# Kernel optimization log

Measured on AMD Instinct MI355X. Metric: run time of the kernel, lower is better.

The kernel has to match this reference:

```python
import jax, jax.numpy as jnp
import numpy as np

P = 8  # patch_size hard-coded in the module


def conv1x1(x, W, b):
    # x: [B,C,H,W_], W: [O,C], b: [O]  (1x1 conv == per-pixel linear)
    return jnp.einsum('oc,bchw->bohw', W, x) + b[None, :, None, None]


def to_patch_tokens(t):
    # Replicates t.unfold(2,P,P).unfold(3,P,P).contiguous().view(B,-1,N)
    # t: [B,Cq,W,H] -> [B, Cq*P*P, N] with N = (W//P)*(H//P)
    B, Cq, Wd, Hd = t.shape
    Wp, Hp = Wd // P, Hd // P
    t = t.reshape(B, Cq, Wp, P, Hp, P).transpose(0, 1, 2, 4, 3, 5)  # [B,Cq,Wp,Hp,P,P]
    return t.reshape(B, Cq * P * P, Wp * Hp)


def setup_inputs() -> dict:
    key = jax.random.key(0)
    ks = jax.random.split(key, 10)
    B, C, Wd, Hd = 8, 64, 256, 256
    Cq = C // 8
    s_in = 1.0 / np.sqrt(C)
    s_out = 1.0 / np.sqrt(Cq)
    return {
        'x': jax.random.normal(ks[0], (B, C, Wd, Hd), jnp.float32),
        'Wq': jax.random.normal(ks[1], (Cq, C), jnp.float32) * s_in,
        'bq': jax.random.normal(ks[2], (Cq,), jnp.float32) * 0.01,
        'Wk': jax.random.normal(ks[3], (Cq, C), jnp.float32) * s_in,
        'bk': jax.random.normal(ks[4], (Cq,), jnp.float32) * 0.01,
        'Wv': jax.random.normal(ks[5], (Cq, C), jnp.float32) * s_in,
        'bv': jax.random.normal(ks[6], (Cq,), jnp.float32) * 0.01,
        'Wo': jax.random.normal(ks[7], (C, Cq), jnp.float32) * s_out,
        'bo': jax.random.normal(ks[8], (C,), jnp.float32) * 0.01,
        'gamma': jax.random.normal(ks[9], (1,), jnp.float32),
    }


def reference(x, Wq, bq, Wk, bk, Wv, bv, Wo, bo, gamma):
    B, C, Wd, Hd = x.shape
    Cq = C // 8
    q = to_patch_tokens(conv1x1(x, Wq, bq)).transpose(0, 2, 1)  # [B,N,M]
    k = to_patch_tokens(conv1x1(x, Wk, bk))                     # [B,M,N]
    v = to_patch_tokens(conv1x1(x, Wv, bv))                     # [B,M,N]
    N = k.shape[-1]  # d_k in source == number of patch tokens
    energy = jnp.einsum('bnm,bmk->bnk', q, k) / jnp.sqrt(jnp.float32(N))
    attn = jax.nn.softmax(energy, axis=-1)                      # [B,N,N]
    out = jnp.einsum('bmn,bjn->bmj', v, attn)                   # bmm(v, attn^T)
    out = out.transpose(0, 2, 1).reshape(B, Cq, Wd, Hd)
    out = conv1x1(out, Wo, bo)
    return gamma * out + x
```

## Files before the change

### kernel.cpp

```cpp
#include <hip/hip_runtime.h>
#include <stdint.h>

typedef unsigned short u16;
typedef unsigned int   u32;
typedef __attribute__((ext_vector_type(8))) short  short8;
typedef __attribute__((ext_vector_type(4))) float  floatx4;

__device__ __forceinline__ u16 f32_to_bf16(float f) {
  u32 u = __builtin_bit_cast(u32, f);
  u = (u + 0x7fffu + ((u >> 16) & 1u)) >> 16;
  return (u16)u;
}
__device__ __forceinline__ float bf16_to_f32(u16 h) {
  u32 u = ((u32)h) << 16;
  return __builtin_bit_cast(float, u);
}

__device__ __forceinline__ void load_lds16(const u16* g, u16* l) {
  auto gp = (const __attribute__((address_space(1))) u32*)(uintptr_t)g;
  auto lp = (__attribute__((address_space(3))) u32*)(u32)(uintptr_t)l;
  __builtin_amdgcn_global_load_lds(gp, lp, 16, 0, 0);
}

__global__ __launch_bounds__(1024) void qkv_kernel(
    const float* __restrict__ x,
    const float* __restrict__ Wq, const float* __restrict__ bq,
    const float* __restrict__ Wk, const float* __restrict__ bk,
    const float* __restrict__ Wv, const float* __restrict__ bv,
    u16* __restrict__ qt, u16* __restrict__ kt, u16* __restrict__ vm)
{
  __shared__ __align__(16) u16 qs[128 * 64];
  __shared__ __align__(16) u16 ks_[128 * 64];
  __shared__ __align__(16) u16 vs[64 * 128];

  const int wq = blockIdx.x;
  const int g  = blockIdx.y;
  const int b  = blockIdx.z;
  const int t  = threadIdx.x;
  const int lw = t >> 5, lh = t & 31;
  const int w  = wq * 32 + lw;
  const int h  = g * 16 + (lh & 15) + ((lh >> 4) << 7);
  const int nl = ((lh >> 3) & 1) * 64 + (lw & 7) * 8 + (lh & 7);
  const int mc = ((lw >> 3) << 1) + (lh >> 4);

  float aq[8], ak[8], av[8];
#pragma unroll
  for (int i = 0; i < 8; i++) { aq[i] = 0.f; ak[i] = 0.f; av[i] = 0.f; }

  const float* xp = x + (size_t)b * 64 * 65536 + w * 256 + h;
#pragma unroll 4
  for (int c = 0; c < 64; c++) {
    float xv = xp[c * 65536];
#pragma unroll
    for (int cq = 0; cq < 8; cq++) {
      aq[cq] = fmaf(Wq[cq * 64 + c], xv, aq[cq]);
      ak[cq] = fmaf(Wk[cq * 64 + c], xv, ak[cq]);
      av[cq] = fmaf(Wv[cq * 64 + c], xv, av[cq]);
    }
  }
#pragma unroll
  for (int cq = 0; cq < 8; cq++) {
    qs[nl * 64 + cq * 8 + mc]  = f32_to_bf16(aq[cq] + bq[cq]);
    ks_[nl * 64 + cq * 8 + mc] = f32_to_bf16(ak[cq] + bk[cq]);
    vs[(cq * 8 + mc) * 128 + nl] = f32_to_bf16(av[cq] + bv[cq]);
  }
  __syncthreads();

  {
    const int nl2 = t >> 3, cq2 = t & 7;
    const size_t row = (size_t)b * 1024 + g * 128 + nl2;
    uint4 vq = *(const uint4*)(qs + nl2 * 64 + cq2 * 8);
    uint4 vk = *(const uint4*)(ks_ + nl2 * 64 + cq2 * 8);
    *(uint4*)(qt + row * 512 + cq2 * 64 + wq * 8) = vq;
    *(uint4*)(kt + row * 512 + cq2 * 64 + wq * 8) = vk;
  }
  {
    const int pr = t >> 4, l16 = t & 15;
    const int cq3 = pr >> 3, mc3 = pr & 7;
    const int mrow = cq3 * 64 + wq * 8 + mc3;
    uint4 vv = *(const uint4*)(vs + pr * 128 + l16 * 8);
    *(uint4*)(vm + ((size_t)b * 512 + mrow) * 1024 + g * 128 + l16 * 8) = vv;
  }
}

template <int FMW>
__global__ __launch_bounds__(256) void gemm_nt(
    const u16* __restrict__ A, const u16* __restrict__ Bm, u16* __restrict__ Cm,
    int M, int N, int K, float scale)
{
  constexpr int BM = FMW * 32;
  __shared__ __align__(16) u16 As[BM * 64];
  __shared__ __align__(16) u16 Bs[128 * 64];

  const int bn = blockIdx.x, bm = blockIdx.y, bz = blockIdx.z;
  const int t = threadIdx.x;
  const int lane = t & 63, wid = t >> 6;
  const int wm = wid & 1, wn = wid >> 1;
  const int m0 = bm * BM, n0 = bn * 128;

  const u16* Ab = A + (size_t)bz * M * K + (size_t)m0 * K;
  const u16* Bb = Bm + (size_t)bz * N * K + (size_t)n0 * K;

  floatx4 acc[FMW][4];
#pragma unroll
  for (int i = 0; i < FMW; i++)
#pragma unroll
    for (int j = 0; j < 4; j++) acc[i][j] = (floatx4){0.f, 0.f, 0.f, 0.f};

  const int srow = wid * 8 + (lane >> 3);
  const int scol = (((lane & 7) ^ ((lane >> 3) & 7)) << 3);
  const int l15 = lane & 15, quad = lane >> 4;
  const int cxor = (l15 & 7) << 3;

  for (int k0 = 0; k0 < K; k0 += 64) {
#pragma unroll
    for (int i = 0; i < FMW; i++)
      load_lds16(Ab + (size_t)(i * 32 + srow) * K + k0 + scol, As + (i * 32 + wid * 8) * 64);
#pragma unroll
    for (int i = 0; i < 4; i++)
      load_lds16(Bb + (size_t)(i * 32 + srow) * K + k0 + scol, Bs + (i * 32 + wid * 8) * 64);
    __syncthreads();
#pragma unroll
    for (int ks = 0; ks < 2; ks++) {
      const int koff = (ks * 32 + quad * 8) ^ cxor;
      short8 a[FMW], b[4];
#pragma unroll
      for (int f = 0; f < FMW; f++)
        a[f] = *(const short8*)(As + (wm * FMW * 16 + f * 16 + l15) * 64 + koff);
#pragma unroll
      for (int f = 0; f < 4; f++)
        b[f] = *(const short8*)(Bs + (wn * 64 + f * 16 + l15) * 64 + koff);
#pragma unroll
      for (int fm = 0; fm < FMW; fm++)
#pragma unroll
        for (int fn = 0; fn < 4; fn++)
          acc[fm][fn] = __builtin_amdgcn_mfma_f32_16x16x32_bf16(a[fm], b[fn], acc[fm][fn], 0, 0, 0);
    }
    __syncthreads();
  }

  u16* Cb = Cm + (size_t)bz * M * N;
#pragma unroll
  for (int fm = 0; fm < FMW; fm++)
#pragma unroll
    for (int fn = 0; fn < 4; fn++)
#pragma unroll
      for (int r = 0; r < 4; r++) {
        int row = m0 + wm * FMW * 16 + fm * 16 + quad * 4 + r;
        int col = n0 + wn * 64 + fn * 16 + l15;
        Cb[(size_t)row * N + col] = f32_to_bf16(scale * acc[fm][fn][r]);
      }
}

__global__ __launch_bounds__(256) void softmax_kernel(u16* __restrict__ EP)
{
  const int r = blockIdx.x;
  u16* row = EP + (size_t)r * 1024;
  const int t = threadIdx.x;
  const int lane = t & 63, wid = t >> 6;

  ushort4 hv = ((const ushort4*)row)[t];
  float e[4] = {bf16_to_f32(hv.x), bf16_to_f32(hv.y), bf16_to_f32(hv.z), bf16_to_f32(hv.w)};

  float mx = fmaxf(fmaxf(e[0], e[1]), fmaxf(e[2], e[3]));
#pragma unroll
  for (int off = 32; off > 0; off >>= 1) mx = fmaxf(mx, __shfl_xor(mx, off));
  __shared__ float redm[4];
  if (lane == 0) redm[wid] = mx;
  __syncthreads();
  mx = fmaxf(fmaxf(redm[0], redm[1]), fmaxf(redm[2], redm[3]));

  float s = 0.f;
#pragma unroll
  for (int i = 0; i < 4; i++) { e[i] = __expf(e[i] - mx); s += e[i]; }
#pragma unroll
  for (int off = 32; off > 0; off >>= 1) s += __shfl_xor(s, off);
  __shared__ float reds[4];
  if (lane == 0) reds[wid] = s;
  __syncthreads();
  s = reds[0] + reds[1] + reds[2] + reds[3];

  float inv = 1.0f / s;
  hv.x = f32_to_bf16(e[0] * inv);
  hv.y = f32_to_bf16(e[1] * inv);
  hv.z = f32_to_bf16(e[2] * inv);
  hv.w = f32_to_bf16(e[3] * inv);
  ((ushort4*)row)[t] = hv;
}

__global__ __launch_bounds__(256) void out_kernel(
    const float* __restrict__ x, const u16* __restrict__ OT,
    const float* __restrict__ Wo, const float* __restrict__ bo,
    const float* __restrict__ gammap, float* __restrict__ out)
{
  const int pix = blockIdx.x * 256 + threadIdx.x;
  const int b = pix >> 16, rem = pix & 65535;
  const float g = gammap[0];

  const u16* otb = OT + (size_t)b * 524288;
  const int m = rem & 511;
  const int nbase = rem >> 9;
  float oc[8];
#pragma unroll
  for (int cq = 0; cq < 8; cq++)
    oc[cq] = bf16_to_f32(otb[(size_t)(cq * 128 + nbase) * 512 + m]);

  const float* xb = x + (size_t)b * 4194304 + rem;
  float* ob = out + (size_t)b * 4194304 + rem;
#pragma unroll 4
  for (int o = 0; o < 64; o++) {
    float acc = bo[o];
#pragma unroll
    for (int cq = 0; cq < 8; cq++) acc = fmaf(Wo[o * 8 + cq], oc[cq], acc);
    ob[o * 65536] = fmaf(g, acc, xb[o * 65536]);
  }
}

extern "C" void kernel_launch(void* const* d_in, const int* in_sizes, int n_in,
                              void* d_out, int out_size, void* d_ws, size_t ws_size,
                              hipStream_t stream) {
  const float* x  = (const float*)d_in[0];
  const float* Wq = (const float*)d_in[1];
  const float* bq = (const float*)d_in[2];
  const float* Wk = (const float*)d_in[3];
  const float* bk = (const float*)d_in[4];
  const float* Wv = (const float*)d_in[5];
  const float* bv = (const float*)d_in[6];
  const float* Wo = (const float*)d_in[7];
  const float* bo = (const float*)d_in[8];
  const float* gm = (const float*)d_in[9];
  float* out = (float*)d_out;

  u16* qt = (u16*)d_ws;
  u16* kt = qt + 4194304;
  u16* vm = kt + 4194304;
  u16* EP = vm + 4194304;
  u16* OT = qt;

  qkv_kernel<<<dim3(8, 8, 8), 1024, 0, stream>>>(x, Wq, bq, Wk, bk, Wv, bv, qt, kt, vm);
  gemm_nt<4><<<dim3(8, 8, 8), 256, 0, stream>>>(qt, kt, EP, 1024, 1024, 512, 0.03125f);
  softmax_kernel<<<8192, 256, 0, stream>>>(EP);
  gemm_nt<2><<<dim3(4, 16, 8), 256, 0, stream>>>(EP, vm, OT, 1024, 512, 1024, 1.0f);
  out_kernel<<<2048, 256, 0, stream>>>(x, OT, Wo, bo, gm, out);
}
```

Before: 340.7 us.

## Fuse five kernels into one persistent kernel with software grid barriers

Replaces the five separate launches with a single persistent kernel of 512 blocks that runs the QKV, energy GEMM, softmax, PV GEMM and output phases in turn, separated by atomic-counter grid barriers. The goal is to remove launch gaps and kernel-boundary drain between stages. The QKV phase now uses 256 threads looping four times, and the first GEMM switches to a 64-row tile done twice per block. This relies on all 512 blocks being co-resident, which could deadlock if occupancy is too low, and the barrier spinning plus reduced per-phase parallelism may cost throughput.

```diff
diff --git a/kernel.cpp b/kernel.cpp
--- a/kernel.cpp
+++ b/kernel.cpp
@@ -22,88 +22,105 @@
   __builtin_amdgcn_global_load_lds(gp, lp, 16, 0, 0);
 }
 
-__global__ __launch_bounds__(1024) void qkv_kernel(
-    const float* __restrict__ x,
+__global__ void init_ctr(u32* ctr) { if (threadIdx.x < 16) ctr[threadIdx.x] = 0; }
+
+__device__ __forceinline__ void grid_barrier(u32* ctr, u32 target) {
+  __syncthreads();
+  if (threadIdx.x == 0) {
+    __threadfence();
+    __hip_atomic_fetch_add(ctr, 1u, __ATOMIC_ACQ_REL, __HIP_MEMORY_SCOPE_AGENT);
+    while (__hip_atomic_load(ctr, __ATOMIC_ACQUIRE, __HIP_MEMORY_SCOPE_AGENT) < target)
+      __builtin_amdgcn_s_sleep(2);
+    __threadfence();
+  }
+  __syncthreads();
+}
+
+__device__ __forceinline__ void qkv_phase(
+    char* pool, int bx, int t, const float* __restrict__ x,
     const float* __restrict__ Wq, const float* __restrict__ bq,
     const float* __restrict__ Wk, const float* __restrict__ bk,
     const float* __restrict__ Wv, const float* __restrict__ bv,
     u16* __restrict__ qt, u16* __restrict__ kt, u16* __restrict__ vm)
 {
-  __shared__ __align__(16) u16 qs[128 * 64];
-  __shared__ __align__(16) u16 ks_[128 * 64];
-  __shared__ __align__(16) u16 vs[64 * 128];
-
-  const int wq = blockIdx.x;
-  const int g  = blockIdx.y;
-  const int b  = blockIdx.z;
-  const int t  = threadIdx.x;
-  const int lw = t >> 5, lh = t & 31;
-  const int w  = wq * 32 + lw;
-  const int h  = g * 16 + (lh & 15) + ((lh >> 4) << 7);
-  const int nl = ((lh >> 3) & 1) * 64 + (lw & 7) * 8 + (lh & 7);
-  const int mc = ((lw >> 3) << 1) + (lh >> 4);
-
-  float aq[8], ak[8], av[8];
-#pragma unroll
-  for (int i = 0; i < 8; i++) { aq[i] = 0.f; ak[i] = 0.f; av[i] = 0.f; }
-
-  const float* xp = x + (size_t)b * 64 * 65536 + w * 256 + h;
+  u16* qs  = (u16*)pool;
+  u16* ks_ = qs + 8192;
+  u16* vs  = ks_ + 8192;
+
+  const int wq = bx & 7, g = (bx >> 3) & 7, b = bx >> 6;
+
+#pragma unroll
+  for (int i = 0; i < 4; i++) {
+    const int vt = t + i * 256;
+    const int lw = vt >> 5, lh = vt & 31;
+    const int w  = wq * 32 + lw;
+    const int h  = g * 16 + (lh & 15) + ((lh >> 4) << 7);
+    const int nl = ((lh >> 3) & 1) * 64 + (lw & 7) * 8 + (lh & 7);
+    const int mc = ((lw >> 3) << 1) + (lh >> 4);
+
+    float aq[8], ak[8], av[8];
+#pragma unroll
+    for (int j = 0; j < 8; j++) { aq[j] = 0.f; ak[j] = 0.f; av[j] = 0.f; }
+
+    const float* xp = x + (size_t)b * 64 * 65536 + w * 256 + h;
 #pragma unroll 4
-  for (int c = 0; c < 64; c++) {
-    float xv = xp[c * 65536];
+    for (int c = 0; c < 64; c++) {
+      float xv = xp[c * 65536];
+#pragma unroll
+      for (int cq = 0; cq < 8; cq++) {
+        aq[cq] = fmaf(Wq[cq * 64 + c], xv, aq[cq]);
+        ak[cq] = fmaf(Wk[cq * 64 + c], xv, ak[cq]);
+        av[cq] = fmaf(Wv[cq * 64 + c], xv, av[cq]);
+      }
+    }
 #pragma unroll
     for (int cq = 0; cq < 8; cq++) {
-      aq[cq] = fmaf(Wq[cq * 64 + c], xv, aq[cq]);
-      ak[cq] = fmaf(Wk[cq * 64 + c], xv, ak[cq]);
-      av[cq] = fmaf(Wv[cq * 64 + c], xv, av[cq]);
-    }
-  }
-#pragma unroll
-  for (int cq = 0; cq < 8; cq++) {
-    qs[nl * 64 + cq * 8 + mc]  = f32_to_bf16(aq[cq] + bq[cq]);
-    ks_[nl * 64 + cq * 8 + mc] = f32_to_bf16(ak[cq] + bk[cq]);
-    vs[(cq * 8 + mc) * 128 + nl] = f32_to_bf16(av[cq] + bv[cq]);
-  }
-  __syncthreads();
-
-  {
-    const int nl2 = t >> 3, cq2 = t & 7;
-    const size_t row = (size_t)b * 1024 + g * 128 + nl2;
-    uint4 vq = *(const uint4*)(qs + nl2 * 64 + cq2 * 8);
-    uint4 vk = *(const uint4*)(ks_ + nl2 * 64 + cq2 * 8);
-    *(uint4*)(qt + row * 512 + cq2 * 64 + wq * 8) = vq;
-    *(uint4*)(kt + row * 512 + cq2 * 64 + wq * 8) = vk;
-  }
-  {
-    const int pr = t >> 4, l16 = t & 15;
-    const int cq3 = pr >> 3, mc3 = pr & 7;
-    const int mrow = cq3 * 64 + wq * 8 + mc3;
-    uint4 vv = *(const uint4*)(vs + pr * 128 + l16 * 8);
-    *(uint4*)(vm + ((size_t)b * 512 + mrow) * 1024 + g * 128 + l16 * 8) = vv;
-  }
-}
-
-template <int FMW>
-__global__ __launch_bounds__(256) void gemm_nt(
+      qs[nl * 64 + cq * 8 + mc]    = f32_to_bf16(aq[cq] + bq[cq]);
+      ks_[nl * 64 + cq * 8 + mc]   = f32_to_bf16(ak[cq] + bk[cq]);
+      vs[(cq * 8 + mc) * 128 + nl] = f32_to_bf16(av[cq] + bv[cq]);
+    }
+  }
+  __syncthreads();
+
+#pragma unroll
+  for (int i = 0; i < 4; i++) {
+    const int vt = t + i * 256;
+    {
+      const int nl2 = vt >> 3, cq2 = vt & 7;
+      const size_t row = (size_t)b * 1024 + g * 128 + nl2;
+      uint4 vq = *(const uint4*)(qs + nl2 * 64 + cq2 * 8);
+      uint4 vk = *(const uint4*)(ks_ + nl2 * 64 + cq2 * 8);
+      *(uint4*)(qt + row * 512 + cq2 * 64 + wq * 8) = vq;
+      *(uint4*)(kt + row * 512 + cq2 * 64 + wq * 8) = vk;
+    }
+    {
+      const int pr = vt >> 4, l16 = vt & 15;
+      const int cq3 = pr >> 3, mc3 = pr & 7;
+      const int mrow = cq3 * 64 + wq * 8 + mc3;
+      uint4 vv = *(const uint4*)(vs + pr * 128 + l16 * 8);
+      *(uint4*)(vm + ((size_t)b * 512 + mrow) * 1024 + g * 128 + l16 * 8) = vv;
+    }
+  }
+}
+
+__device__ __forceinline__ void gemm_phase(
+    char* pool, int t,
     const u16* __restrict__ A, const u16* __restrict__ Bm, u16* __restrict__ Cm,
-    int M, int N, int K, float scale)
-{
-  constexpr int BM = FMW * 32;
-  __shared__ __align__(16) u16 As[BM * 64];
-  __shared__ __align__(16) u16 Bs[128 * 64];
-
-  const int bn = blockIdx.x, bm = blockIdx.y, bz = blockIdx.z;
-  const int t = threadIdx.x;
+    int M, int N, int K, float scale, int bm, int bn, int bz)
+{
+  u16* As = (u16*)pool;
+  u16* Bs = As + 4096;
+
   const int lane = t & 63, wid = t >> 6;
   const int wm = wid & 1, wn = wid >> 1;
-  const int m0 = bm * BM, n0 = bn * 128;
+  const int m0 = bm * 64, n0 = bn * 128;
 
   const u16* Ab = A + (size_t)bz * M * K + (size_t)m0 * K;
   const u16* Bb = Bm + (size_t)bz * N * K + (size_t)n0 * K;
 
-  floatx4 acc[FMW][4];
-#pragma unroll
-  for (int i = 0; i < FMW; i++)
+  floatx4 acc[2][4];
+#pragma unroll
+  for (int i = 0; i < 2; i++)
 #pragma unroll
     for (int j = 0; j < 4; j++) acc[i][j] = (floatx4){0.f, 0.f, 0.f, 0.f};
 
@@ -114,7 +131,7 @@
 
   for (int k0 = 0; k0 < K; k0 += 64) {
 #pragma unroll
-    for (int i = 0; i < FMW; i++)
+    for (int i = 0; i < 2; i++)
       load_lds16(Ab + (size_t)(i * 32 + srow) * K + k0 + scol, As + (i * 32 + wid * 8) * 64);
 #pragma unroll
     for (int i = 0; i < 4; i++)
@@ -123,15 +140,15 @@
 #pragma unroll
     for (int ks = 0; ks < 2; ks++) {
       const int koff = (ks * 32 + quad * 8) ^ cxor;
-      short8 a[FMW], b[4];
-#pragma unroll
-      for (int f = 0; f < FMW; f++)
-        a[f] = *(const short8*)(As + (wm * FMW * 16 + f * 16 + l15) * 64 + koff);
+      short8 a[2], b[4];
+#pragma unroll
+      for (int f = 0; f < 2; f++)
+        a[f] = *(const short8*)(As + (wm * 32 + f * 16 + l15) * 64 + koff);
 #pragma unroll
       for (int f = 0; f < 4; f++)
         b[f] = *(const short8*)(Bs + (wn * 64 + f * 16 + l15) * 64 + koff);
 #pragma unroll
-      for (int fm = 0; fm < FMW; fm++)
+      for (int fm = 0; fm < 2; fm++)
 #pragma unroll
         for (int fn = 0; fn < 4; fn++)
           acc[fm][fn] = __builtin_amdgcn_mfma_f32_16x16x32_bf16(a[fm], b[fn], acc[fm][fn], 0, 0, 0);
@@ -141,22 +158,21 @@
 
   u16* Cb = Cm + (size_t)bz * M * N;
 #pragma unroll
-  for (int fm = 0; fm < FMW; fm++)
+  for (int fm = 0; fm < 2; fm++)
 #pragma unroll
     for (int fn = 0; fn < 4; fn++)
 #pragma unroll
       for (int r = 0; r < 4; r++) {
-        int row = m0 + wm * FMW * 16 + fm * 16 + quad * 4 + r;
+        int row = m0 + wm * 32 + fm * 16 + quad * 4 + r;
         int col = n0 + wn * 64 + fn * 16 + l15;
         Cb[(size_t)row * N + col] = f32_to_bf16(scale * acc[fm][fn][r]);
       }
 }
 
-__global__ __launch_bounds__(256) void softmax_kernel(u16* __restrict__ EP)
-{
-  const int r = blockIdx.x;
-  u16* row = EP + (size_t)r * 1024;
-  const int t = threadIdx.x;
+__device__ __forceinline__ void softmax_row(char* pool, int t, u16* __restrict__ row)
+{
+  float* redm = (float*)pool;
+  float* reds = redm + 4;
   const int lane = t & 63, wid = t >> 6;
 
   ushort4 hv = ((const ushort4*)row)[t];
@@ -165,7 +181,6 @@
   float mx = fmaxf(fmaxf(e[0], e[1]), fmaxf(e[2], e[3]));
 #pragma unroll
   for (int off = 32; off > 0; off >>= 1) mx = fmaxf(mx, __shfl_xor(mx, off));
-  __shared__ float redm[4];
   if (lane == 0) redm[wid] = mx;
   __syncthreads();
   mx = fmaxf(fmaxf(redm[0], redm[1]), fmaxf(redm[2], redm[3]));
@@ -175,7 +190,6 @@
   for (int i = 0; i < 4; i++) { e[i] = __expf(e[i] - mx); s += e[i]; }
 #pragma unroll
   for (int off = 32; off > 0; off >>= 1) s += __shfl_xor(s, off);
-  __shared__ float reds[4];
   if (lane == 0) reds[wid] = s;
   __syncthreads();
   s = reds[0] + reds[1] + reds[2] + reds[3];
@@ -188,15 +202,12 @@
   ((ushort4*)row)[t] = hv;
 }
 
-__global__ __launch_bounds__(256) void out_kernel(
-    const float* __restrict__ x, const u16* __restrict__ OT,
+__device__ __forceinline__ void out_phase(
+    int pix, const float* __restrict__ x, const u16* __restrict__ OT,
     const float* __restrict__ Wo, const float* __restrict__ bo,
-    const float* __restrict__ gammap, float* __restrict__ out)
-{
-  const int pix = blockIdx.x * 256 + threadIdx.x;
+    float g, float* __restrict__ out)
+{
   const int b = pix >> 16, rem = pix & 65535;
-  const float g = gammap[0];
-
   const u16* otb = OT + (size_t)b * 524288;
   const int m = rem & 511;
   const int nbase = rem >> 9;
@@ -213,6 +224,50 @@
 #pragma unroll
     for (int cq = 0; cq < 8; cq++) acc = fmaf(Wo[o * 8 + cq], oc[cq], acc);
     ob[o * 65536] = fmaf(g, acc, xb[o * 65536]);
+  }
+}
+
+__global__ __launch_bounds__(256, 2) void mega_kernel(
+    const float* __restrict__ x,
+    const float* __restrict__ Wq, const float* __restrict__ bq,
+    const float* __restrict__ Wk, const float* __restrict__ bk,
+    const float* __restrict__ Wv, const float* __restrict__ bv,
+    const float* __restrict__ Wo, const float* __restrict__ bo,
+    const float* __restrict__ gammap,
+    u16* __restrict__ qt, u16* __restrict__ kt, u16* __restrict__ vm,
+    u16* __restrict__ EP, u32* __restrict__ ctr, float* __restrict__ out)
+{
+  __shared__ __align__(16) char pool[49152];
+  const int bx = blockIdx.x, t = threadIdx.x;
+  u16* OT = qt;
+
+  qkv_phase(pool, bx, t, x, Wq, bq, Wk, bk, Wv, bv, qt, kt, vm);
+  grid_barrier(ctr + 0, 512);
+
+#pragma unroll 1
+  for (int rep = 0; rep < 2; rep++) {
+    int job = bx + 512 * rep;
+    gemm_phase(pool, t, qt, kt, EP, 1024, 1024, 512, 0.03125f,
+               (job >> 3) & 15, job & 7, job >> 7);
+  }
+  grid_barrier(ctr + 1, 512);
+
+#pragma unroll 1
+  for (int j = 0; j < 16; j++) {
+    softmax_row(pool, t, EP + (size_t)(bx * 16 + j) * 1024);
+    __syncthreads();
+  }
+  grid_barrier(ctr + 2, 512);
+
+  gemm_phase(pool, t, EP, vm, OT, 1024, 512, 1024, 1.0f,
+             (bx >> 2) & 15, bx & 3, bx >> 6);
+  grid_barrier(ctr + 3, 512);
+
+  const float g = gammap[0];
+#pragma unroll 1
+  for (int rep = 0; rep < 4; rep++) {
+    int pix = (bx + 512 * rep) * 256 + t;
+    out_phase(pix, x, OT, Wo, bo, g, out);
   }
 }
 
@@ -235,11 +290,9 @@
   u16* kt = qt + 4194304;
   u16* vm = kt + 4194304;
   u16* EP = vm + 4194304;
-  u16* OT = qt;
-
-  qkv_kernel<<<dim3(8, 8, 8), 1024, 0, stream>>>(x, Wq, bq, Wk, bk, Wv, bv, qt, kt, vm);
-  gemm_nt<4><<<dim3(8, 8, 8), 256, 0, stream>>>(qt, kt, EP, 1024, 1024, 512, 0.03125f);
-  softmax_kernel<<<8192, 256, 0, stream>>>(EP);
-  gemm_nt<2><<<dim3(4, 16, 8), 256, 0, stream>>>(EP, vm, OT, 1024, 512, 1024, 1.0f);
-  out_kernel<<<2048, 256, 0, stream>>>(x, OT, Wo, bo, gm, out);
-}
+  u32* ctr = (u32*)((char*)d_ws + 41943040);
+
+  init_ctr<<<1, 16, 0, stream>>>(ctr);
+  mega_kernel<<<512, 256, 0, stream>>>(x, Wq, bq, Wk, bk, Wv, bv, Wo, bo, gm,
+                                       qt, kt, vm, EP, ctr, out);
+}
```

Measured after the change: 685.2 us. 101% more time.
